# Kernel optimization log

Hardware: AMD Instinct MI355X
Metric: run time of the kernel (lower is better)

The kernel has to match this reference:

```python
import jax, jax.numpy as jnp
import numpy as np

N_NODES = 100000
N_EDGES = 2000000
D = 128
HIDDEN = 128


def setup_inputs() -> dict:
    key = jax.random.key(0)
    k_src, k_dst, k_idx, k_w1, k_w2 = jax.random.split(key, 5)
    src = jax.random.normal(k_src, (N_NODES, D), dtype=jnp.float32)
    dst = jax.random.normal(k_dst, (N_NODES, D), dtype=jnp.float32)
    edge_label_index = jax.random.randint(k_idx, (2, N_EDGES), 0, N_NODES, dtype=jnp.int64)
    # Kaiming-ish init for the two linear layers
    W1 = jax.random.normal(k_w1, (D, HIDDEN), dtype=jnp.float32) / np.sqrt(D)
    b1 = jnp.zeros((HIDDEN,), dtype=jnp.float32)
    W2 = jax.random.normal(k_w2, (HIDDEN, 1), dtype=jnp.float32) / np.sqrt(HIDDEN)
    b2 = jnp.zeros((1,), dtype=jnp.float32)
    return {"src": src, "dst": dst, "edge_label_index": edge_label_index,
            "W1": W1, "b1": b1, "W2": W2, "b2": b2}


def reference(src, dst, edge_label_index, W1, b1, W2, b2):
    row = edge_label_index[0]
    col = edge_label_index[1]
    # gather endpoint embeddings and fuse with elementwise product: [E, D]
    z = src[row] * dst[col]
    # 2-layer MLP; dropout p=0 is the identity
    h = jax.nn.relu(z @ W1 + b1)           # [E, HIDDEN]
    out = h @ W2 + b2                       # [E, 1]
    return out.reshape(-1)                  # [E]
```

## Files before the change

### kernel.cpp

```cpp
#include <hip/hip_runtime.h>
#include <hip/hip_bf16.h>
#include <hip/hip_fp16.h>

typedef __attribute__((ext_vector_type(8))) _Float16 half8;
typedef __attribute__((ext_vector_type(4))) float f32x4;

#define BLOCK 256
#define GTILE 16
#define NBKT  32

__device__ __forceinline__ int swz16(int row, int boff) {
    return (row << 8) + (boff ^ ((row & 15) << 4));
}
__device__ __forceinline__ int swzH(int row, int boff) {
    return (row << 7) + (boff ^ ((row & 7) << 4));
}

__device__ __forceinline__ int probe_i64(const int* eli) {
    int any = 0;
    #pragma unroll
    for (int i = 0; i < 32; ++i) any |= eli[2 * i + 1];
    return (any == 0) ? 1 : 0;
}

__global__ __launch_bounds__(256) void cvt_hist_kernel(
    const float* __restrict__ a, const float* __restrict__ b,
    _Float16* __restrict__ oa, _Float16* __restrict__ ob, int n,
    const int* __restrict__ eli, int E, float scale, unsigned int* __restrict__ cnt)
{
    __shared__ unsigned int h[NBKT];
    __shared__ int s_i64;
    if (threadIdx.x < NBKT) h[threadIdx.x] = 0;
    if (threadIdx.x == 0) s_i64 = probe_i64(eli);
    __syncthreads();

    const int i = blockIdx.x * blockDim.x + threadIdx.x;
    const int stride = gridDim.x * blockDim.x;
    const float4* a4 = (const float4*)a;
    const float4* b4 = (const float4*)b;
    const int n8 = n >> 3;
    for (int j = i; j < n8; j += stride) {
        float4 x0 = a4[2 * j], x1 = a4[2 * j + 1];
        float4 y0 = b4[2 * j], y1 = b4[2 * j + 1];
        union { _Float16 hh[8]; uint4 u; } pa, pb;
        pa.hh[0]=(_Float16)x0.x; pa.hh[1]=(_Float16)x0.y;
        pa.hh[2]=(_Float16)x0.z; pa.hh[3]=(_Float16)x0.w;
        pa.hh[4]=(_Float16)x1.x; pa.hh[5]=(_Float16)x1.y;
        pa.hh[6]=(_Float16)x1.z; pa.hh[7]=(_Float16)x1.w;
        pb.hh[0]=(_Float16)y0.x; pb.hh[1]=(_Float16)y0.y;
        pb.hh[2]=(_Float16)y0.z; pb.hh[3]=(_Float16)y0.w;
        pb.hh[4]=(_Float16)y1.x; pb.hh[5]=(_Float16)y1.y;
        pb.hh[6]=(_Float16)y1.z; pb.hh[7]=(_Float16)y1.w;
        ((uint4*)oa)[j] = pa.u;
        ((uint4*)ob)[j] = pb.u;
    }
    for (int j = (n8 << 3) + i; j < n; j += stride) {
        oa[j] = (_Float16)a[j];
        ob[j] = (_Float16)b[j];
    }
    const int i64f = s_i64;
    for (int e = i; e < E; e += stride) {
        int c = i64f ? eli[2 * ((size_t)E + e)] : eli[(size_t)E + e];
        int bkt = (int)((float)c * scale);
        if (bkt > NBKT - 1) bkt = NBKT - 1;
        atomicAdd(&h[bkt], 1u);
    }
    __syncthreads();
    if (threadIdx.x < NBKT && h[threadIdx.x])
        atomicAdd(&cnt[threadIdx.x], h[threadIdx.x]);
}

__global__ void scan_kernel(const unsigned int* __restrict__ cnt,
                            unsigned int* __restrict__ segStart,
                            unsigned int* __restrict__ cursor)
{
    if (threadIdx.x == 0) {
        unsigned int s = 0;
        for (int b = 0; b < NBKT; ++b) { segStart[b] = s; cursor[b] = s; s += cnt[b]; }
        segStart[NBKT] = s;
    }
}

__global__ __launch_bounds__(256) void scatter_kernel(
    const int* __restrict__ eli, int E, float scale,
    unsigned int* __restrict__ cursor, uint2* __restrict__ sorted)
{
    __shared__ unsigned int lcnt[NBKT];
    __shared__ unsigned int lpos[NBKT];
    __shared__ int s_i64;
    if (threadIdx.x < NBKT) lcnt[threadIdx.x] = 0;
    if (threadIdx.x == 0) s_i64 = probe_i64(eli);
    __syncthreads();
    const int i64f = s_i64;

    const int chunk = (E + gridDim.x - 1) / gridDim.x;
    const int e0 = blockIdx.x * chunk;
    const int e1 = min(E, e0 + chunk);

    for (int e = e0 + threadIdx.x; e < e1; e += blockDim.x) {
        int c = i64f ? eli[2 * ((size_t)E + e)] : eli[(size_t)E + e];
        int bkt = (int)((float)c * scale);
        if (bkt > NBKT - 1) bkt = NBKT - 1;
        atomicAdd(&lcnt[bkt], 1u);
    }
    __syncthreads();
    if (threadIdx.x < NBKT) {
        unsigned int nv = lcnt[threadIdx.x];
        lpos[threadIdx.x] = nv ? atomicAdd(&cursor[threadIdx.x], nv) : 0u;
    }
    __syncthreads();
    for (int e = e0 + threadIdx.x; e < e1; e += blockDim.x) {
        int r, c;
        if (i64f) { r = eli[2 * (size_t)e]; c = eli[2 * ((size_t)E + e)]; }
        else      { r = eli[e];             c = eli[(size_t)E + e]; }
        int bkt = (int)((float)c * scale);
        if (bkt > NBKT - 1) bkt = NBKT - 1;
        unsigned int pos = atomicAdd(&lpos[bkt], 1u);
        unsigned lo = (unsigned)r | ((unsigned)c << 17);
        unsigned hi = ((unsigned)c >> 15) | ((unsigned)e << 2);
        sorted[pos] = make_uint2(lo, hi);
    }
}

__global__ __launch_bounds__(BLOCK, 3) void mlp_sorted_kernel(
    const _Float16* __restrict__ srcb, const _Float16* __restrict__ dstb,
    const uint2* __restrict__ sorted, const unsigned int* __restrict__ segStart,
    const float* __restrict__ W1, const float* __restrict__ b1,
    const float* __restrict__ W2, const float* __restrict__ b2,
    float* __restrict__ out, int E)
{
    __shared__ __align__(16) char lds[49152];

    const int tid  = threadIdx.x;
    const int lane = tid & 63;
    const int w    = tid >> 6;
    const int rr   = lane & 15;
    const int kgrp = lane >> 4;
    const int rq8  = lane >> 3;
    const int cl   = lane & 7;

    for (int idx = tid; idx < 128 * 128; idx += BLOCK) {
        int k = idx >> 7, n = idx & 127;
        *(_Float16*)(lds + swz16(n, k * 2)) = (_Float16)W1[idx];
    }
    __syncthreads();

    char* zb = lds + 32768 + (w << 12);

    float b1s[8], w2s[8];
    #pragma unroll
    for (int cb = 0; cb < 8; ++cb) {
        b1s[cb] = b1[cb * 16 + rr];
        w2s[cb] = W2[cb * 16 + rr];
    }
    const float bias2 = b2[0];

    const int x     = blockIdx.x & 7;
    const int kb    = blockIdx.x >> 3;
    const int nbs   = gridDim.x >> 3;
    const int wslot = kb * 4 + w;
    const int wstep = nbs * 4;

    const half8* s8 = (const half8*)srcb;
    const half8* d8 = (const half8*)dstb;

    half8 svA[4], dvA[4], svB[4], dvB[4];
    int eoA = 0, eoB = 0;
    int s0 = 0, s1 = 0;

    auto loadT = [&](int t, half8 (&s)[4], half8 (&d)[4], int& eo) {
        int idx = s0 + t * 16 + rr; if (idx >= s1) idx = s1 - 1;
        uint2 pk = sorted[idx];
        int r = (int)(pk.x & 0x1FFFFu);
        int c = (int)(((pk.x >> 17) | (pk.y << 15)) & 0x1FFFFu);
        eo = (int)(pk.y >> 2);
        #pragma unroll
        for (int i = 0; i < 4; ++i) {
            int hr = i * 8 + rq8, e = hr >> 1, hh = hr & 1;
            int rn = __shfl(r, e, 64);
            int cn = __shfl(c, e, 64);
            s[i] = s8[(size_t)rn * 16 + hh * 8 + cl];
            d[i] = d8[(size_t)cn * 16 + hh * 8 + cl];
        }
    };
    auto writeZ = [&](const half8 (&s)[4], const half8 (&d)[4]) {
        #pragma unroll
        for (int i = 0; i < 4; ++i) {
            int hr = i * 8 + rq8;
            half8 pr = s[i] * d[i];
            *(half8*)(zb + swzH(hr, cl * 16)) = pr;
        }
    };
    auto compute = [&](int base, int eoCur) {
        int cnt = s1 - base; if (cnt > 16) cnt = 16;
        f32x4 acc[8];
        #pragma unroll
        for (int cb = 0; cb < 8; ++cb) acc[cb] = (f32x4){0.f, 0.f, 0.f, 0.f};
        __builtin_amdgcn_s_setprio(1);
        #pragma unroll
        for (int kk = 0; kk < 4; ++kk) {
            half8 af = *(const half8*)(zb + swzH(rr * 2 + (kk >> 1),
                                                 (kk & 1) * 64 + kgrp * 16));
            #pragma unroll
            for (int cb = 0; cb < 8; ++cb) {
                half8 bf = *(const half8*)(lds + swz16(cb * 16 + rr,
                                                       kk * 64 + kgrp * 16));
                acc[cb] = __builtin_amdgcn_mfma_f32_16x16x32_f16(af, bf, acc[cb], 0, 0, 0);
            }
        }
        __builtin_amdgcn_s_setprio(0);
        #pragma unroll
        for (int r = 0; r < 4; ++r) {
            float p = 0.f;
            #pragma unroll
            for (int cb = 0; cb < 8; ++cb) {
                float hv = acc[cb][r] + b1s[cb];
                hv = fmaxf(hv, 0.f);
                p = fmaf(hv, w2s[cb], p);
            }
            p += __shfl_xor(p, 1, 64);
            p += __shfl_xor(p, 2, 64);
            p += __shfl_xor(p, 4, 64);
            p += __shfl_xor(p, 8, 64);
            int es = kgrp * 4 + r;
            int eOrig = __shfl(eoCur, es, 64);
            if (rr == 0 && es < cnt)
                out[eOrig] = p + bias2;
        }
    };

    for (int j = 0; j < NBKT / 8; ++j) {
        const int b = x + 8 * j;
        s0 = (int)segStart[b];
        s1 = (int)segStart[b + 1];
        if (s1 <= s0) continue;
        const int nt = (s1 - s0 + 15) >> 4;
        int t = wslot;
        if (t >= nt) continue;

        loadT(t, svA, dvA, eoA);
        if (t + wstep < nt) loadT(t + wstep, svB, dvB, eoB);

        while (true) {
            asm volatile("" ::: "memory");
            writeZ(svA, dvA);
            int eoCur = eoA;
            int tp = t + 2 * wstep;
            if (tp < nt) loadT(tp, svA, dvA, eoA);
            asm volatile("" ::: "memory");
            compute(s0 + t * 16, eoCur);
            t += wstep; if (t >= nt) break;

            asm volatile("" ::: "memory");
            writeZ(svB, dvB);
            eoCur = eoB;
            tp = t + 2 * wstep;
            if (tp < nt) loadT(tp, svB, dvB, eoB);
            asm volatile("" ::: "memory");
            compute(s0 + t * 16, eoCur);
            t += wstep; if (t >= nt) break;
        }
    }
}

template<int MODE>
__global__ __launch_bounds__(BLOCK, 3) void edge_mlp_fb(
    const float* __restrict__ srcf, const float* __restrict__ dstf,
    const _Float16* __restrict__ srcb, const _Float16* __restrict__ dstb,
    const int* __restrict__ eli,
    const float* __restrict__ W1, const float* __restrict__ b1,
    const float* __restrict__ W2, const float* __restrict__ b2,
    float* __restrict__ out, int E)
{
    __shared__ __align__(16) char lds[49152];
    const int tid  = threadIdx.x;
    const int lane = tid & 63;
    const int w    = tid >> 6;
    const int rr   = lane & 15;
    const int kgrp = lane >> 4;
    const int rq8  = lane >> 3;
    const int cl   = lane & 7;

    for (int idx = tid; idx < 128 * 128; idx += BLOCK) {
        int k = idx >> 7, n = idx & 127;
        *(_Float16*)(lds + swz16(n, k * 2)) = (_Float16)W1[idx];
    }
    int probe = eli[2 * (lane & 31) + 1];
    unsigned long long bl = __ballot(lane < 32 && probe != 0);
    const int i64f = (bl == 0ull) ? 1 : 0;
    __syncthreads();

    char* zb = lds + 32768 + (w << 12);
    float b1s[8], w2s[8];
    #pragma unroll
    for (int cb = 0; cb < 8; ++cb) {
        b1s[cb] = b1[cb * 16 + rr];
        w2s[cb] = W2[cb * 16 + rr];
    }
    const float bias2 = b2[0];

    const int ngroups = (E + GTILE - 1) / GTILE;
    const int step = gridDim.x * 4;
    int g = blockIdx.x * 4 + w;
    if (g >= ngroups) return;

    auto idxload = [&](int gg) -> int {
        gg = gg < ngroups ? gg : ngroups - 1;
        int e = gg * GTILE + rr; if (e >= E) e = E - 1;
        size_t off = (lane < 32) ? (size_t)e : (size_t)E + (size_t)e;
        return i64f ? eli[2 * off] : eli[off];
    };

    half8 sv[4], dv[4];
    auto loadT = [&](int iv) {
        const half8* s8 = (const half8*)srcb;
        const half8* d8 = (const half8*)dstb;
        #pragma unroll
        for (int i = 0; i < 4; ++i) {
            int hr = i * 8 + rq8, e = hr >> 1, hh = hr & 1;
            int r = __shfl(iv, e, 64);
            int c = __shfl(iv, 32 + e, 64);
            sv[i] = s8[(size_t)r * 16 + hh * 8 + cl];
            dv[i] = d8[(size_t)c * 16 + hh * 8 + cl];
        }
    };
    auto stageF = [&](int iv) {
        const float4* s4 = (const float4*)srcf;
        const float4* d4 = (const float4*)dstf;
        #pragma unroll
        for (int i = 0; i < 4; ++i) {
            int hr = i * 8 + rq8, e = hr >> 1, hh = hr & 1;
            int r = __shfl(iv, e, 64);
            int c = __shfl(iv, 32 + e, 64);
            float4 a0 = s4[(size_t)r * 32 + hh * 16 + cl * 2];
            float4 a1 = s4[(size_t)r * 32 + hh * 16 + cl * 2 + 1];
            float4 c0 = d4[(size_t)c * 32 + hh * 16 + cl * 2];
            float4 c1 = d4[(size_t)c * 32 + hh * 16 + cl * 2 + 1];
            union { _Float16 hf[8]; half8 v; } pr;
            pr.hf[0]=(_Float16)(a0.x*c0.x); pr.hf[1]=(_Float16)(a0.y*c0.y);
            pr.hf[2]=(_Float16)(a0.z*c0.z); pr.hf[3]=(_Float16)(a0.w*c0.w);
            pr.hf[4]=(_Float16)(a1.x*c1.x); pr.hf[5]=(_Float16)(a1.y*c1.y);
            pr.hf[6]=(_Float16)(a1.z*c1.z); pr.hf[7]=(_Float16)(a1.w*c1.w);
            *(half8*)(zb + swzH(hr, cl * 16)) = pr.v;
        }
    };
    auto compute = [&](int gg) {
        f32x4 acc[8];
        #pragma unroll
        for (int cb = 0; cb < 8; ++cb) acc[cb] = (f32x4){0.f, 0.f, 0.f, 0.f};
        __builtin_amdgcn_s_setprio(1);
        #pragma unroll
        for (int kk = 0; kk < 4; ++kk) {
            half8 af = *(const half8*)(zb + swzH(rr * 2 + (kk >> 1),
                                                 (kk & 1) * 64 + kgrp * 16));
            #pragma unroll
            for (int cb = 0; cb < 8; ++cb) {
                half8 bf = *(const half8*)(lds + swz16(cb * 16 + rr,
                                                       kk * 64 + kgrp * 16));
                acc[cb] = __builtin_amdgcn_mfma_f32_16x16x32_f16(af, bf, acc[cb], 0, 0, 0);
            }
        }
        __builtin_amdgcn_s_setprio(0);
        #pragma unroll
        for (int r = 0; r < 4; ++r) {
            float p = 0.f;
            #pragma unroll
            for (int cb = 0; cb < 8; ++cb) {
                float hv = acc[cb][r] + b1s[cb];
                hv = fmaxf(hv, 0.f);
                p = fmaf(hv, w2s[cb], p);
            }
            p += __shfl_xor(p, 1, 64);
            p += __shfl_xor(p, 2, 64);
            p += __shfl_xor(p, 4, 64);
            p += __shfl_xor(p, 8, 64);
            int e = gg * GTILE + kgrp * 4 + r;
            if (rr == 0 && e < E) out[e] = p + bias2;
        }
    };

    if constexpr (MODE == 1) {
        int iv = idxload(g);
        loadT(iv);
        while (true) {
            asm volatile("" ::: "memory");
            #pragma unroll
            for (int i = 0; i < 4; ++i) {
                int hr = i * 8 + rq8;
                half8 pr = sv[i] * dv[i];
                *(half8*)(zb + swzH(hr, cl * 16)) = pr;
            }
            int gn = g + step;
            if (gn < ngroups) { int iv2 = idxload(gn); loadT(iv2); }
            asm volatile("" ::: "memory");
            compute(g);
            if (gn >= ngroups) break;
            g = gn;
        }
    } else {
        for (; g < ngroups; g += step) {
            asm volatile("" ::: "memory");
            int iv = idxload(g);
            stageF(iv);
            asm volatile("" ::: "memory");
            compute(g);
        }
    }
}

extern "C" void kernel_launch(void* const* d_in, const int* in_sizes, int n_in,
                              void* d_out, int out_size, void* d_ws, size_t ws_size,
                              hipStream_t stream) {
    const float* src = (const float*)d_in[0];
    const float* dst = (const float*)d_in[1];
    const int*   eli = (const int*)d_in[2];
    const float* W1  = (const float*)d_in[3];
    const float* b1  = (const float*)d_in[4];
    const float* W2  = (const float*)d_in[5];
    const float* b2  = (const float*)d_in[6];
    float* out = (float*)d_out;

    const int E = in_sizes[2] / 2;
    const int n = in_sizes[0];
    const int N = n / 128;
    const float scale = (float)NBKT / (float)N;

    const size_t NB = (size_t)n * sizeof(_Float16);
    const size_t need_full = 4096 + 2 * NB + (size_t)E * 8;
    const size_t need_tab  = 2 * NB + 4096;
    const bool packable = (N <= 131072) && (E < (1 << 29));

    if (ws_size >= need_full && packable) {
        char* wsb = (char*)d_ws;
        unsigned int* cnt      = (unsigned int*)wsb;
        unsigned int* segStart = cnt + 32;
        unsigned int* cursor   = segStart + 40;
        _Float16* srcb = (_Float16*)(wsb + 4096);
        _Float16* dstb = srcb + n;
        uint2* sorted  = (uint2*)(wsb + 4096 + 2 * NB);

        hipMemsetAsync(wsb, 0, 4096, stream);
        cvt_hist_kernel<<<dim3(2048), dim3(256), 0, stream>>>(
            src, dst, srcb, dstb, n, eli, E, scale, cnt);
        scan_kernel<<<dim3(1), dim3(64), 0, stream>>>(cnt, segStart, cursor);
        scatter_kernel<<<dim3(256), dim3(256), 0, stream>>>(
            eli, E, scale, cursor, sorted);
        mlp_sorted_kernel<<<dim3(768), dim3(BLOCK), 0, stream>>>(
            srcb, dstb, sorted, segStart, W1, b1, W2, b2, out, E);
    } else if (ws_size >= need_tab) {
        char* wsb = (char*)d_ws;
        unsigned int* cnt = (unsigned int*)(wsb + 2 * NB);
        _Float16* sb = (_Float16*)wsb;
        _Float16* db = sb + n;
        hipMemsetAsync(cnt, 0, 4096, stream);
        cvt_hist_kernel<<<dim3(2048), dim3(256), 0, stream>>>(
            src, dst, sb, db, n, eli, E, scale, cnt);
        const int ngroups = (E + GTILE - 1) / GTILE;
        int nblocks = (ngroups + 3) / 4;
        int grid = nblocks < 768 ? nblocks : 768;
        edge_mlp_fb<1><<<dim3(grid), dim3(BLOCK), 0, stream>>>(
            src, dst, sb, db, eli, W1, b1, W2, b2, out, E);
    } else {
        const int ngroups = (E + GTILE - 1) / GTILE;
        int nblocks = (ngroups + 3) / 4;
        int grid = nblocks < 768 ? nblocks : 768;
        edge_mlp_fb<0><<<dim3(grid), dim3(BLOCK), 0, stream>>>(
            src, dst, (const _Float16*)nullptr, (const _Float16*)nullptr,
            eli, W1, b1, W2, b2, out, E);
    }
}
```

Before: 206.0 us.

## Write MLP outputs in sorted order and permute back in separate kernel

The scatter kernel now stores unpacked (row, col) pairs plus an inverse permutation, and the sorted MLP kernel writes results contiguously to a temp buffer instead of scattering to original edge positions. A new permute kernel gathers the temp buffer back into output order. The MLP kernel also moves to 512-thread blocks with 8 waves and 64KB LDS on a 512-block grid. This aims to replace scattered 4-byte output writes with coalesced ones, at the cost of extra workspace traffic (inv, tmp, wider sorted entries) and one more launch.

```diff
diff --git a/kernel.cpp b/kernel.cpp
--- a/kernel.cpp
+++ b/kernel.cpp
@@ -5,7 +5,6 @@
 typedef __attribute__((ext_vector_type(8))) _Float16 half8;
 typedef __attribute__((ext_vector_type(4))) float f32x4;
 
-#define BLOCK 256
 #define GTILE 16
 #define NBKT  32
 
@@ -83,7 +82,8 @@
 
 __global__ __launch_bounds__(256) void scatter_kernel(
     const int* __restrict__ eli, int E, float scale,
-    unsigned int* __restrict__ cursor, uint2* __restrict__ sorted)
+    unsigned int* __restrict__ cursor,
+    uint2* __restrict__ sorted, unsigned int* __restrict__ inv)
 {
     __shared__ unsigned int lcnt[NBKT];
     __shared__ unsigned int lpos[NBKT];
@@ -116,20 +116,19 @@
         int bkt = (int)((float)c * scale);
         if (bkt > NBKT - 1) bkt = NBKT - 1;
         unsigned int pos = atomicAdd(&lpos[bkt], 1u);
-        unsigned lo = (unsigned)r | ((unsigned)c << 17);
-        unsigned hi = ((unsigned)c >> 15) | ((unsigned)e << 2);
-        sorted[pos] = make_uint2(lo, hi);
-    }
-}
-
-__global__ __launch_bounds__(BLOCK, 3) void mlp_sorted_kernel(
+        sorted[pos] = make_uint2((unsigned)r, (unsigned)c);
+        inv[e] = pos;
+    }
+}
+
+__global__ __launch_bounds__(512, 4) void mlp_sorted_kernel(
     const _Float16* __restrict__ srcb, const _Float16* __restrict__ dstb,
     const uint2* __restrict__ sorted, const unsigned int* __restrict__ segStart,
     const float* __restrict__ W1, const float* __restrict__ b1,
     const float* __restrict__ W2, const float* __restrict__ b2,
-    float* __restrict__ out, int E)
-{
-    __shared__ __align__(16) char lds[49152];
+    float* __restrict__ tmp, int E)
+{
+    __shared__ __align__(16) char lds[65536];
 
     const int tid  = threadIdx.x;
     const int lane = tid & 63;
@@ -139,7 +138,7 @@
     const int rq8  = lane >> 3;
     const int cl   = lane & 7;
 
-    for (int idx = tid; idx < 128 * 128; idx += BLOCK) {
+    for (int idx = tid; idx < 128 * 128; idx += 512) {
         int k = idx >> 7, n = idx & 127;
         *(_Float16*)(lds + swz16(n, k * 2)) = (_Float16)W1[idx];
     }
@@ -158,27 +157,23 @@
     const int x     = blockIdx.x & 7;
     const int kb    = blockIdx.x >> 3;
     const int nbs   = gridDim.x >> 3;
-    const int wslot = kb * 4 + w;
-    const int wstep = nbs * 4;
+    const int wslot = kb * 8 + w;
+    const int wstep = nbs * 8;
 
     const half8* s8 = (const half8*)srcb;
     const half8* d8 = (const half8*)dstb;
 
     half8 svA[4], dvA[4], svB[4], dvB[4];
-    int eoA = 0, eoB = 0;
     int s0 = 0, s1 = 0;
 
-    auto loadT = [&](int t, half8 (&s)[4], half8 (&d)[4], int& eo) {
+    auto loadT = [&](int t, half8 (&s)[4], half8 (&d)[4]) {
         int idx = s0 + t * 16 + rr; if (idx >= s1) idx = s1 - 1;
-        uint2 pk = sorted[idx];
-        int r = (int)(pk.x & 0x1FFFFu);
-        int c = (int)(((pk.x >> 17) | (pk.y << 15)) & 0x1FFFFu);
-        eo = (int)(pk.y >> 2);
+        uint2 iv = sorted[idx];
         #pragma unroll
         for (int i = 0; i < 4; ++i) {
             int hr = i * 8 + rq8, e = hr >> 1, hh = hr & 1;
-            int rn = __shfl(r, e, 64);
-            int cn = __shfl(c, e, 64);
+            int rn = __shfl((int)iv.x, e, 64);
+            int cn = __shfl((int)iv.y, e, 64);
             s[i] = s8[(size_t)rn * 16 + hh * 8 + cl];
             d[i] = d8[(size_t)cn * 16 + hh * 8 + cl];
         }
@@ -191,7 +186,7 @@
             *(half8*)(zb + swzH(hr, cl * 16)) = pr;
         }
     };
-    auto compute = [&](int base, int eoCur) {
+    auto compute = [&](int base) {
         int cnt = s1 - base; if (cnt > 16) cnt = 16;
         f32x4 acc[8];
         #pragma unroll
@@ -223,9 +218,8 @@
             p += __shfl_xor(p, 4, 64);
             p += __shfl_xor(p, 8, 64);
             int es = kgrp * 4 + r;
-            int eOrig = __shfl(eoCur, es, 64);
             if (rr == 0 && es < cnt)
-                out[eOrig] = p + bias2;
+                tmp[base + es] = p + bias2;
         }
     };
 
@@ -238,33 +232,40 @@
         int t = wslot;
         if (t >= nt) continue;
 
-        loadT(t, svA, dvA, eoA);
-        if (t + wstep < nt) loadT(t + wstep, svB, dvB, eoB);
+        loadT(t, svA, dvA);
+        if (t + wstep < nt) loadT(t + wstep, svB, dvB);
 
         while (true) {
             asm volatile("" ::: "memory");
             writeZ(svA, dvA);
-            int eoCur = eoA;
             int tp = t + 2 * wstep;
-            if (tp < nt) loadT(tp, svA, dvA, eoA);
-            asm volatile("" ::: "memory");
-            compute(s0 + t * 16, eoCur);
+            if (tp < nt) loadT(tp, svA, dvA);
+            asm volatile("" ::: "memory");
+            compute(s0 + t * 16);
             t += wstep; if (t >= nt) break;
 
             asm volatile("" ::: "memory");
             writeZ(svB, dvB);
-            eoCur = eoB;
             tp = t + 2 * wstep;
-            if (tp < nt) loadT(tp, svB, dvB, eoB);
-            asm volatile("" ::: "memory");
-            compute(s0 + t * 16, eoCur);
+            if (tp < nt) loadT(tp, svB, dvB);
+            asm volatile("" ::: "memory");
+            compute(s0 + t * 16);
             t += wstep; if (t >= nt) break;
         }
     }
 }
 
+__global__ __launch_bounds__(256) void permute_kernel(
+    const float* __restrict__ tmp, const unsigned int* __restrict__ inv,
+    float* __restrict__ out, int E)
+{
+    for (int e = blockIdx.x * blockDim.x + threadIdx.x; e < E;
+         e += gridDim.x * blockDim.x)
+        out[e] = tmp[inv[e]];
+}
+
 template<int MODE>
-__global__ __launch_bounds__(BLOCK, 3) void edge_mlp_fb(
+__global__ __launch_bounds__(256, 3) void edge_mlp_fb(
     const float* __restrict__ srcf, const float* __restrict__ dstf,
     const _Float16* __restrict__ srcb, const _Float16* __restrict__ dstb,
     const int* __restrict__ eli,
@@ -281,7 +282,7 @@
     const int rq8  = lane >> 3;
     const int cl   = lane & 7;
 
-    for (int idx = tid; idx < 128 * 128; idx += BLOCK) {
+    for (int idx = tid; idx < 128 * 128; idx += 256) {
         int k = idx >> 7, n = idx & 127;
         *(_Float16*)(lds + swz16(n, k * 2)) = (_Float16)W1[idx];
     }
@@ -426,11 +427,10 @@
     const float scale = (float)NBKT / (float)N;
 
     const size_t NB = (size_t)n * sizeof(_Float16);
-    const size_t need_full = 4096 + 2 * NB + (size_t)E * 8;
+    const size_t need_full = 4096 + 2 * NB + (size_t)E * 16;
     const size_t need_tab  = 2 * NB + 4096;
-    const bool packable = (N <= 131072) && (E < (1 << 29));
-
-    if (ws_size >= need_full && packable) {
+
+    if (ws_size >= need_full) {
         char* wsb = (char*)d_ws;
         unsigned int* cnt      = (unsigned int*)wsb;
         unsigned int* segStart = cnt + 32;
@@ -438,15 +438,18 @@
         _Float16* srcb = (_Float16*)(wsb + 4096);
         _Float16* dstb = srcb + n;
         uint2* sorted  = (uint2*)(wsb + 4096 + 2 * NB);
+        unsigned int* inv = (unsigned int*)(sorted + E);
+        float* tmp = (float*)(inv + E);
 
         hipMemsetAsync(wsb, 0, 4096, stream);
         cvt_hist_kernel<<<dim3(2048), dim3(256), 0, stream>>>(
             src, dst, srcb, dstb, n, eli, E, scale, cnt);
         scan_kernel<<<dim3(1), dim3(64), 0, stream>>>(cnt, segStart, cursor);
         scatter_kernel<<<dim3(256), dim3(256), 0, stream>>>(
-            eli, E, scale, cursor, sorted);
-        mlp_sorted_kernel<<<dim3(768), dim3(BLOCK), 0, stream>>>(
-            srcb, dstb, sorted, segStart, W1, b1, W2, b2, out, E);
+            eli, E, scale, cursor, sorted, inv);
+        mlp_sorted_kernel<<<dim3(512), dim3(512), 0, stream>>>(
+            srcb, dstb, sorted, segStart, W1, b1, W2, b2, tmp, E);
+        permute_kernel<<<dim3(2048), dim3(256), 0, stream>>>(tmp, inv, out, E);
     } else if (ws_size >= need_tab) {
         char* wsb = (char*)d_ws;
         unsigned int* cnt = (unsigned int*)(wsb + 2 * NB);
@@ -458,13 +461,13 @@
         const int ngroups = (E + GTILE - 1) / GTILE;
         int nblocks = (ngroups + 3) / 4;
         int grid = nblocks < 768 ? nblocks : 768;
-        edge_mlp_fb<1><<<dim3(grid), dim3(BLOCK), 0, stream>>>(
+        edge_mlp_fb<1><<<dim3(grid), dim3(256), 0, stream>>>(
             src, dst, sb, db, eli, W1, b1, W2, b2, out, E);
     } else {
         const int ngroups = (E + GTILE - 1) / GTILE;
         int nblocks = (ngroups + 3) / 4;
         int grid = nblocks < 768 ? nblocks : 768;
-        edge_mlp_fb<0><<<dim3(grid), dim3(BLOCK), 0, stream>>>(
+        edge_mlp_fb<0><<<dim3(grid), dim3(256), 0, stream>>>(
             src, dst, (const _Float16*)nullptr, (const _Float16*)nullptr,
             eli, W1, b1, W2, b2, out, E);
     }
```

After: 355.1 us. 1.72x slower.
